# Kernel optimization log

Hardware: AMD Instinct MI355X
Metric: run time of the kernel (lower is better)

The kernel has to match this reference:

```python
import jax, jax.numpy as jnp
import numpy as np

IGNORE_INDEX = -100
EPS = 1e-8


def setup_inputs() -> dict:
    key = jax.random.key(0)
    k1, k2, k3 = jax.random.split(key, 3)
    B, S, D, V = 2, 4096, 1024, 32000
    outputs = jax.random.normal(k1, (B, S, D), dtype=jnp.float32)
    proj_weight = jax.random.normal(k2, (V, D), dtype=jnp.float32) * (D ** -0.5)
    targets = jax.random.randint(k3, (B, S), 0, V)
    # mark a prefix of each sequence as ignored (e.g. prompt tokens)
    targets = targets.at[:, :128].set(IGNORE_INDEX)
    targets = targets.astype(jnp.int64) if jax.config.jax_enable_x64 else targets.astype(jnp.int32)
    return {"outputs": outputs, "proj_weight": proj_weight, "targets": targets}


def reference(outputs, proj_weight, targets):
    # outputs: [B, S, D]; proj_weight: [V, D]; targets: [B, S]
    valid = targets != IGNORE_INDEX                              # [B, S]
    # sqrt-length token weights: 1/sqrt(num_valid_in_row), zero on ignored
    l_values = valid.sum(axis=1, keepdims=True).astype(jnp.float32)
    weights = valid.astype(jnp.float32) / jnp.sqrt(l_values + EPS)  # [B, S]

    logits = jnp.einsum('bsd,vd->bsv', outputs, proj_weight).astype(jnp.float32)
    logp = jax.nn.log_softmax(logits, axis=-1)                   # [B, S, V]
    safe_tgt = jnp.where(valid, targets, 0)
    token_losses = -jnp.take_along_axis(logp, safe_tgt[..., None], axis=-1)[..., 0]
    token_losses = jnp.where(valid, token_losses, 0.0)           # CE with ignore_index

    total_weighted_loss = jnp.sum(token_losses * weights)
    total_weights = jnp.sum(weights)
    return jnp.where(total_weights == 0, total_weighted_loss,
                     total_weighted_loss / total_weights)
```

## Files before the change

### kernel.cpp

```cpp
#include <hip/hip_runtime.h>
#include <hip/hip_bf16.h>
#include <math.h>

#define IGNORE_INDEX (-100)
#define BB 2
#define SS 4096
#define MM (BB * SS)
#define DD 1024
#define VV 32000

#define BM 128
#define BN 128
#define BKT 32
#define NCHUNK (2 * (VV / BN))
#define NWG ((MM / BM) * (VV / BN))

typedef __attribute__((ext_vector_type(8))) short bf16x8;
typedef __attribute__((ext_vector_type(4))) float f32x4;

__device__ __forceinline__ void gload_lds16(const void* g, void* l) {
  __builtin_amdgcn_global_load_lds((const __attribute__((address_space(1))) void*)g,
                                   (__attribute__((address_space(3))) void*)l,
                                   16, 0, 0);
}

__device__ __forceinline__ short f2bf(float f) {
  unsigned u = __float_as_uint(f);
  u += 0x7fffu + ((u >> 16) & 1u);
  return (short)(u >> 16);
}

__device__ __forceinline__ float bf2f(short s) {
  return __uint_as_float(((unsigned)(unsigned short)s) << 16);
}

__global__ void cvt_bf16_kernel(const float* __restrict__ src, short* __restrict__ dst, int n4) {
  int i = blockIdx.x * blockDim.x + threadIdx.x;
  if (i >= n4) return;
  const float4 f = ((const float4*)src)[i];
  short4 o;
  o.x = f2bf(f.x); o.y = f2bf(f.y); o.z = f2bf(f.z); o.w = f2bf(f.w);
  ((short4*)dst)[i] = o;
}

__global__ void count_kernel(const int* __restrict__ tgt, float* __restrict__ counts) {
  __shared__ int red[256];
  int b = blockIdx.x;
  int c = 0;
  for (int s = threadIdx.x; s < SS; s += 256) c += (tgt[b * SS + s] != IGNORE_INDEX) ? 1 : 0;
  red[threadIdx.x] = c;
  __syncthreads();
  for (int off = 128; off > 0; off >>= 1) {
    if (threadIdx.x < off) red[threadIdx.x] += red[threadIdx.x + off];
    __syncthreads();
  }
  if (threadIdx.x == 0) counts[b] = (float)red[0];
}

__global__ __launch_bounds__(256) void gemm_lse_kernel(
    const short* __restrict__ A,
    const short* __restrict__ W,
    float2* __restrict__ partials) {
  __shared__ short sA[BM * BKT];
  __shared__ short sB[BN * BKT];
  const int tid = threadIdx.x;
  const int lane = tid & 63;
  const int wid = tid >> 6;
  const int wr = wid >> 1, wc = wid & 1;

  const int wg = blockIdx.x;
  const int xcdb = wg & 7;
  const int local = wg >> 3;
  const int mt = xcdb * 8 + (local & 7);
  const int nt = local >> 3;

  const int mbase = mt * BM;
  const int nbase = nt * BN;

  const int srow = tid >> 2;
  const int skoff = (tid & 3) << 3;
  const short* Ag = A + (size_t)(mbase + srow) * DD + skoff;
  const short* Bg = W + (size_t)(nbase + srow) * DD + skoff;
  short* sAp = &sA[tid * 8];
  short* sBp = &sB[tid * 8];

  f32x4 acc[4][4] = {};

  const int fr = lane & 15;
  const int fk = (lane >> 4) << 3;
  const short* sAr = &sA[(wr * 64 + fr) * BKT + fk];
  const short* sBr = &sB[(wc * 64 + fr) * BKT + fk];

  for (int kt = 0; kt < DD; kt += BKT) {
    gload_lds16(Ag + kt, sAp);
    gload_lds16(Ag + kt + (size_t)64 * DD, sAp + 2048);
    gload_lds16(Bg + kt, sBp);
    gload_lds16(Bg + kt + (size_t)64 * DD, sBp + 2048);
    __syncthreads();
    bf16x8 a[4], b[4];
#pragma unroll
    for (int m = 0; m < 4; ++m) a[m] = *(const bf16x8*)(sAr + m * 16 * BKT);
#pragma unroll
    for (int n = 0; n < 4; ++n) b[n] = *(const bf16x8*)(sBr + n * 16 * BKT);
#pragma unroll
    for (int m = 0; m < 4; ++m)
#pragma unroll
      for (int n = 0; n < 4; ++n)
        acc[m][n] = __builtin_amdgcn_mfma_f32_16x16x32_bf16(a[m], b[n], acc[m][n], 0, 0, 0);
    __syncthreads();
  }

  const int chunk = nt * 2 + wc;
  const int rowg0 = mbase + wr * 64 + (lane >> 4) * 4;
#pragma unroll
  for (int m = 0; m < 4; ++m) {
#pragma unroll
    for (int i = 0; i < 4; ++i) {
      float v = fmaxf(fmaxf(acc[m][0][i], acc[m][1][i]), fmaxf(acc[m][2][i], acc[m][3][i]));
#pragma unroll
      for (int off = 8; off >= 1; off >>= 1) v = fmaxf(v, __shfl_xor(v, off));
      float s = __expf(acc[m][0][i] - v) + __expf(acc[m][1][i] - v)
              + __expf(acc[m][2][i] - v) + __expf(acc[m][3][i] - v);
#pragma unroll
      for (int off = 8; off >= 1; off >>= 1) s += __shfl_xor(s, off);
      if ((lane & 15) == 0) {
        partials[(size_t)(rowg0 + m * 16 + i) * NCHUNK + chunk] = make_float2(v, s);
      }
    }
  }
}

__global__ void finalize_kernel(const short* __restrict__ A, const short* __restrict__ W,
                                const int* __restrict__ tgt,
                                const float2* __restrict__ partials,
                                const float* __restrict__ counts,
                                float2* __restrict__ tokres) {
  const int gtid = blockIdx.x * blockDim.x + threadIdx.x;
  const int t = gtid >> 6;
  const int lane = gtid & 63;
  if (t >= MM) return;
  const int target = tgt[t];

  float m = -INFINITY, Z = 0.f;
  const float2* p = partials + (size_t)t * NCHUNK;
  for (int c = lane; c < NCHUNK; c += 64) {
    float2 pc = p[c];
    if (pc.x > m) { Z = Z * __expf(m - pc.x) + pc.y; m = pc.x; }
    else          { Z += pc.y * __expf(pc.x - m); }
  }
#pragma unroll
  for (int off = 1; off < 64; off <<= 1) {
    float mo = __shfl_xor(m, off);
    float Zo = __shfl_xor(Z, off);
    float mn = fmaxf(m, mo);
    Z = Z * __expf(m - mn) + Zo * __expf(mo - mn);
    m = mn;
  }

  float dot = 0.f;
  if (target != IGNORE_INDEX) {
    const bf16x8* a8 = (const bf16x8*)(A + (size_t)t * DD) + lane * 2;
    const bf16x8* w8 = (const bf16x8*)(W + (size_t)target * DD) + lane * 2;
#pragma unroll
    for (int j = 0; j < 2; ++j) {
      bf16x8 av = a8[j], wv = w8[j];
#pragma unroll
      for (int e = 0; e < 8; ++e) dot += bf2f(av[e]) * bf2f(wv[e]);
    }
#pragma unroll
    for (int off = 1; off < 64; off <<= 1) dot += __shfl_xor(dot, off);
  }

  if (lane == 0) {
    float wl = 0.f, w = 0.f;
    if (target != IGNORE_INDEX) {
      float l = counts[t >> 12];
      w = 1.0f / sqrtf(l + 1e-8f);
      wl = (m + __logf(Z) - dot) * w;
    }
    tokres[t] = make_float2(wl, w);
  }
}

__global__ void loss_reduce_kernel(const float2* __restrict__ tokres, float* __restrict__ out) {
  __shared__ float sl[256], sw[256];
  float l = 0.f, w = 0.f;
  for (int i = threadIdx.x; i < MM; i += 256) { float2 v = tokres[i]; l += v.x; w += v.y; }
  sl[threadIdx.x] = l; sw[threadIdx.x] = w;
  __syncthreads();
  for (int off = 128; off > 0; off >>= 1) {
    if (threadIdx.x < off) { sl[threadIdx.x] += sl[threadIdx.x + off]; sw[threadIdx.x] += sw[threadIdx.x + off]; }
    __syncthreads();
  }
  if (threadIdx.x == 0) out[0] = (sw[0] == 0.f) ? sl[0] : sl[0] / sw[0];
}

extern "C" void kernel_launch(void* const* d_in, const int* in_sizes, int n_in,
                              void* d_out, int out_size, void* d_ws, size_t ws_size,
                              hipStream_t stream) {
  const float* outputs = (const float*)d_in[0];
  const float* proj    = (const float*)d_in[1];
  const int*   targets = (const int*)d_in[2];
  float* out = (float*)d_out;

  char* base = (char*)d_ws;
  short*  Abf      = (short*)base;
  short*  Wbf      = (short*)(base + (size_t)MM * DD * 2);
  float2* partials = (float2*)(base + (size_t)MM * DD * 2 + (size_t)VV * DD * 2);
  float*  counts   = (float*)((char*)partials + (size_t)MM * NCHUNK * 8);
  float2* tokres   = (float2*)((char*)counts + 256);

  cvt_bf16_kernel<<<(MM * DD / 4) / 256, 256, 0, stream>>>(outputs, Abf, MM * DD / 4);
  cvt_bf16_kernel<<<(VV * DD / 4) / 256, 256, 0, stream>>>(proj, Wbf, VV * DD / 4);
  count_kernel<<<BB, 256, 0, stream>>>(targets, counts);
  gemm_lse_kernel<<<NWG, 256, 0, stream>>>(Abf, Wbf, partials);
  finalize_kernel<<<(MM * 64) / 256, 256, 0, stream>>>(Abf, Wbf, targets, partials, counts, tokres);
  loss_reduce_kernel<<<1, 256, 0, stream>>>(tokres, out);
}
```

Before: 870.8 us.

## Rewrite GEMM-LSE as 256x256 tiles with 4-stage LDS pipeline and swizzle

Replaces the 128x128 single-buffered GEMM with a 256x256 tile, 8-wave kernel that keeps a 4-deep ring of LDS buffers. Global-to-LDS loads are issued two K-steps ahead, with explicit vmcnt/lgkmcnt waits and raised wave priority around the MFMA bursts. An XOR swizzle on the K offset avoids LDS bank conflicts. The goal is to hide load latency and raise arithmetic intensity per tile. In exchange it uses much more LDS and registers per block, which lowers occupancy, and the hand-placed synchronisation is easy to get wrong.

```diff
diff --git a/kernel.cpp b/kernel.cpp
--- a/kernel.cpp
+++ b/kernel.cpp
@@ -9,11 +9,14 @@
 #define DD 1024
 #define VV 32000
 
-#define BM 128
-#define BN 128
-#define BKT 32
-#define NCHUNK (2 * (VV / BN))
-#define NWG ((MM / BM) * (VV / BN))
+#define BM2 256
+#define BN2 256
+#define BK2 32
+#define NT (DD / BK2)
+#define TM_TILES (MM / BM2)
+#define TN_TILES (VV / BN2)
+#define NWG2 (TM_TILES * TN_TILES)
+#define NCHUNK (VV / 64)
 
 typedef __attribute__((ext_vector_type(8))) short bf16x8;
 typedef __attribute__((ext_vector_type(4))) float f32x4;
@@ -29,10 +32,13 @@
   u += 0x7fffu + ((u >> 16) & 1u);
   return (short)(u >> 16);
 }
-
 __device__ __forceinline__ float bf2f(short s) {
   return __uint_as_float(((unsigned)(unsigned short)s) << 16);
 }
+
+#define SBAR() { __builtin_amdgcn_s_barrier(); __builtin_amdgcn_sched_barrier(0); }
+#define WAIT_LGKM0() { asm volatile("s_waitcnt lgkmcnt(0)" ::: "memory"); __builtin_amdgcn_sched_barrier(0); }
+#define WAIT_VMC(N) { asm volatile("s_waitcnt vmcnt(" #N ")" ::: "memory"); __builtin_amdgcn_sched_barrier(0); }
 
 __global__ void cvt_bf16_kernel(const float* __restrict__ src, short* __restrict__ dst, int n4) {
   int i = blockIdx.x * blockDim.x + threadIdx.x;
@@ -57,63 +63,92 @@
   if (threadIdx.x == 0) counts[b] = (float)red[0];
 }
 
-__global__ __launch_bounds__(256) void gemm_lse_kernel(
+__device__ __forceinline__ void read4(const short* p, bf16x8* r) {
+#pragma unroll
+  for (int i = 0; i < 4; ++i) r[i] = *(const bf16x8*)(p + i * 512);
+}
+__device__ __forceinline__ void mfma16(const bf16x8* a4, const bf16x8* b4, f32x4 (*acc4)[4]) {
+#pragma unroll
+  for (int m = 0; m < 4; ++m)
+#pragma unroll
+    for (int n = 0; n < 4; ++n)
+      acc4[m][n] = __builtin_amdgcn_mfma_f32_16x16x32_bf16(a4[m], b4[n], acc4[m][n], 0, 0, 0);
+}
+
+__global__ __launch_bounds__(512, 2) void gemm_lse8_kernel(
     const short* __restrict__ A,
     const short* __restrict__ W,
     float2* __restrict__ partials) {
-  __shared__ short sA[BM * BKT];
-  __shared__ short sB[BN * BKT];
+  __shared__ short sA[4 * 8192];
+  __shared__ short sB[4 * 8192];
   const int tid = threadIdx.x;
   const int lane = tid & 63;
   const int wid = tid >> 6;
-  const int wr = wid >> 1, wc = wid & 1;
+  const int wr = wid >> 2;
+  const int wc = wid & 3;
 
   const int wg = blockIdx.x;
-  const int xcdb = wg & 7;
   const int local = wg >> 3;
-  const int mt = xcdb * 8 + (local & 7);
-  const int nt = local >> 3;
-
-  const int mbase = mt * BM;
-  const int nbase = nt * BN;
+  const int mt = (wg & 7) * 4 + (local & 3);
+  const int nt = local >> 2;
+  const int mbase = mt * BM2;
+  const int nbase = nt * BN2;
 
   const int srow = tid >> 2;
-  const int skoff = (tid & 3) << 3;
-  const short* Ag = A + (size_t)(mbase + srow) * DD + skoff;
-  const short* Bg = W + (size_t)(nbase + srow) * DD + skoff;
-  short* sAp = &sA[tid * 8];
-  short* sBp = &sB[tid * 8];
-
-  f32x4 acc[4][4] = {};
+  const int skoff = ((tid & 3) << 3) ^ (((tid >> 5) & 1) << 4);
+  const short* Asrc = A + (size_t)(mbase + srow) * DD + skoff;
+  const short* Bsrc = W + (size_t)(nbase + srow) * DD + skoff;
 
   const int fr = lane & 15;
-  const int fk = (lane >> 4) << 3;
-  const short* sAr = &sA[(wr * 64 + fr) * BKT + fk];
-  const short* sBr = &sB[(wc * 64 + fr) * BKT + fk];
-
-  for (int kt = 0; kt < DD; kt += BKT) {
-    gload_lds16(Ag + kt, sAp);
-    gload_lds16(Ag + kt + (size_t)64 * DD, sAp + 2048);
-    gload_lds16(Bg + kt, sBp);
-    gload_lds16(Bg + kt + (size_t)64 * DD, sBp + 2048);
-    __syncthreads();
-    bf16x8 a[4], b[4];
-#pragma unroll
-    for (int m = 0; m < 4; ++m) a[m] = *(const bf16x8*)(sAr + m * 16 * BKT);
-#pragma unroll
-    for (int n = 0; n < 4; ++n) b[n] = *(const bf16x8*)(sBr + n * 16 * BKT);
-#pragma unroll
-    for (int m = 0; m < 4; ++m)
-#pragma unroll
-      for (int n = 0; n < 4; ++n)
-        acc[m][n] = __builtin_amdgcn_mfma_f32_16x16x32_bf16(a[m], b[n], acc[m][n], 0, 0, 0);
-    __syncthreads();
-  }
-
-  const int chunk = nt * 2 + wc;
-  const int rowg0 = mbase + wr * 64 + (lane >> 4) * 4;
-#pragma unroll
-  for (int m = 0; m < 4; ++m) {
+  const int kk = ((lane >> 4) << 3) ^ (((lane >> 3) & 1) << 4);
+  const int offA = (wr * 128 + fr) * 32 + kk;
+  const int offB = (wc * 64 + fr) * 32 + kk;
+
+  f32x4 acc[8][4] = {};
+  bf16x8 a[4], b[4];
+
+#define STAGE_AT(tt) { const int _so = ((tt) & 3) * 8192; \
+    const short* _s = Asrc + (size_t)(tt) * BK2; \
+    gload_lds16(_s, &sA[_so + tid * 8]); \
+    gload_lds16(_s + (size_t)128 * DD, &sA[_so + 4096 + tid * 8]); }
+#define STAGE_BT(tt) { const int _so = ((tt) & 3) * 8192; \
+    const short* _s = Bsrc + (size_t)(tt) * BK2; \
+    gload_lds16(_s, &sB[_so + tid * 8]); \
+    gload_lds16(_s + (size_t)128 * DD, &sB[_so + 4096 + tid * 8]); }
+
+  STAGE_AT(0); STAGE_BT(0); STAGE_AT(1); STAGE_BT(1);
+  WAIT_VMC(4);
+  SBAR();
+
+#define TILE(t, DOSTAGE) { \
+    const int bufo = ((t) & 3) * 8192; \
+    read4(&sA[bufo + offA], a); \
+    read4(&sB[bufo + offB], b); \
+    if (DOSTAGE) STAGE_AT((t) + 2); \
+    SBAR(); WAIT_LGKM0(); \
+    __builtin_amdgcn_s_setprio(1); mfma16(a, b, &acc[0]); __builtin_amdgcn_s_setprio(0); \
+    SBAR(); \
+    read4(&sA[bufo + offA + 2048], a); \
+    if (DOSTAGE) STAGE_BT((t) + 2); \
+    SBAR(); WAIT_LGKM0(); \
+    __builtin_amdgcn_s_setprio(1); mfma16(a, b, &acc[4]); __builtin_amdgcn_s_setprio(0); \
+  }
+
+#pragma unroll 1
+  for (int t = 0; t < NT - 2; ++t) {
+    TILE(t, true);
+    WAIT_VMC(4);
+    SBAR();
+  }
+  TILE(NT - 2, false);
+  WAIT_VMC(0);
+  SBAR();
+  TILE(NT - 1, false);
+
+  const int chunk = nt * 4 + wc;
+  const int rowg0 = mbase + wr * 128 + ((lane >> 4) << 2);
+#pragma unroll
+  for (int m = 0; m < 8; ++m) {
 #pragma unroll
     for (int i = 0; i < 4; ++i) {
       float v = fmaxf(fmaxf(acc[m][0][i], acc[m][1][i]), fmaxf(acc[m][2][i], acc[m][3][i]));
@@ -213,7 +248,7 @@
   cvt_bf16_kernel<<<(MM * DD / 4) / 256, 256, 0, stream>>>(outputs, Abf, MM * DD / 4);
   cvt_bf16_kernel<<<(VV * DD / 4) / 256, 256, 0, stream>>>(proj, Wbf, VV * DD / 4);
   count_kernel<<<BB, 256, 0, stream>>>(targets, counts);
-  gemm_lse_kernel<<<NWG, 256, 0, stream>>>(Abf, Wbf, partials);
+  gemm_lse8_kernel<<<NWG2, 512, 0, stream>>>(Abf, Wbf, partials);
   finalize_kernel<<<(MM * 64) / 256, 256, 0, stream>>>(Abf, Wbf, targets, partials, counts, tokres);
   loss_reduce_kernel<<<1, 256, 0, stream>>>(tokres, out);
 }
```

Result: slower. 948.6 us (+8.9%).
